# Performance work log

Hardware: AMD Instinct MI355X
Metric: run time of the kernel (lower is better)

Reference implementation:

```python
import jax, jax.numpy as jnp
import numpy as np

N = 32768      # total nodes = 256 graphs x 128 nodes
G = 256        # graphs in batch
NPG = 128      # nodes per graph
DEG = 8        # incoming edges per node
E = N * DEG    # 262144 edges
F_IN = 64      # node feature size
F_E = 16       # edge feature size
EMB = 64       # out_channels per head == embedding_size
H = 4          # attention heads
HC = H * EMB   # 256
DENSE = 256
K = 64         # ceil(0.5 * NPG)
EPS = 1e-5


def setup_inputs() -> dict:
    key = jax.random.key(0)
    ks = list(jax.random.split(key, 32))
    it = iter(ks)
    s = 0.05

    def rn(shape):
        return jax.random.normal(next(it), shape, jnp.float32) * s

    x = jax.random.normal(next(it), (N, F_IN), jnp.float32)
    dst = jnp.repeat(jnp.arange(N, dtype=jnp.int32), DEG)
    src = (dst // NPG) * NPG + jax.random.randint(next(it), (E,), 0, NPG, dtype=jnp.int32)
    edge_index = jnp.stack([src, dst])                      # [2, E], edges stay within graph
    edge_attr = jax.random.normal(next(it), (E, F_E), jnp.float32)
    batch_index = jnp.arange(N, dtype=jnp.int32) // NPG

    inp = dict(
        x=x, edge_index=edge_index, edge_attr=edge_attr, batch_index=batch_index,
        # TransformerConv 1 (in=F_IN)
        Wq1=rn((F_IN, HC)), bq1=jnp.zeros((HC,), jnp.float32),
        Wk1=rn((F_IN, HC)), bk1=jnp.zeros((HC,), jnp.float32),
        Wv1=rn((F_IN, HC)), bv1=jnp.zeros((HC,), jnp.float32),
        We1=rn((F_E, HC)),
        Ws1=rn((F_IN, HC)), bs1=jnp.zeros((HC,), jnp.float32),
        Wb1=rn((3 * HC, 1)),
        t1_W=rn((HC, EMB)), t1_b=jnp.zeros((EMB,), jnp.float32),
        bn1_g=jnp.ones((EMB,), jnp.float32), bn1_b=jnp.zeros((EMB,), jnp.float32),
        # TransformerConv 2 (in=EMB)
        Wq2=rn((EMB, HC)), bq2=jnp.zeros((HC,), jnp.float32),
        Wk2=rn((EMB, HC)), bk2=jnp.zeros((HC,), jnp.float32),
        Wv2=rn((EMB, HC)), bv2=jnp.zeros((HC,), jnp.float32),
        We2=rn((F_E, HC)),
        Ws2=rn((EMB, HC)), bs2=jnp.zeros((HC,), jnp.float32),
        Wb2=rn((3 * HC, 1)),
        t2_W=rn((HC, EMB)), t2_b=jnp.zeros((EMB,), jnp.float32),
        bn2_g=jnp.ones((EMB,), jnp.float32), bn2_b=jnp.zeros((EMB,), jnp.float32),
        # TopKPooling + MLP head
        pool_w=rn((EMB,)),
        l1_W=rn((2 * EMB, DENSE)), l1_b=jnp.zeros((DENSE,), jnp.float32),
        l2_W=rn((DENSE, DENSE // 2)), l2_b=jnp.zeros((DENSE // 2,), jnp.float32),
        l3_W=rn((DENSE // 2, 1)), l3_b=jnp.zeros((1,), jnp.float32),
    )
    return inp


def _tconv(x, src, dst, ea, Wq, bq, Wk, bk, Wv, bv, We, Ws, bs, Wb):
    """PyG TransformerConv with edge_dim, beta=True, concat=True."""
    n = x.shape[0]
    q = (x @ Wq + bq).reshape(n, H, EMB)                    # [N,H,C]
    eemb = (ea @ We).reshape(-1, H, EMB)                    # [E,H,C]
    k = (x @ Wk + bk)[src].reshape(-1, H, EMB) + eemb       # edge features added to key
    v = (x @ Wv + bv)[src].reshape(-1, H, EMB) + eemb       # and to value
    alpha = jnp.einsum('ehc,ehc->eh', q[dst], k) / jnp.sqrt(jnp.float32(EMB))  # [E,H]
    # stable segment softmax over incoming edges of each dst node
    amax = jax.ops.segment_max(alpha, dst, num_segments=n)
    pexp = jnp.exp(alpha - amax[dst])
    denom = jax.ops.segment_sum(pexp, dst, num_segments=n)
    attn = pexp / denom[dst]                                # [E,H]
    out = jax.ops.segment_sum(v * attn[..., None], dst, num_segments=n).reshape(n, HC)
    # beta gated skip: lin_skip(x) and lin_beta([out, xr, out-xr])
    xr = x @ Ws + bs
    beta = jax.nn.sigmoid(jnp.concatenate([out, xr, out - xr], axis=-1) @ Wb)  # [N,1]
    return beta * xr + (1.0 - beta) * out


def _bn(x, g, b):
    m = x.mean(0)
    v = x.var(0)
    return g * (x - m) * jax.lax.rsqrt(v + EPS) + b


def _forward(x, edge_attr,
             Wq1, bq1, Wk1, bk1, Wv1, bv1, We1, Ws1, bs1, Wb1, t1_W, t1_b, bn1_g, bn1_b,
             Wq2, bq2, Wk2, bk2, Wv2, bv2, We2, Ws2, bs2, Wb2, t2_W, t2_b, bn2_g, bn2_b,
             pool_w, l1_W, l1_b, l2_W, l2_b, l3_W, l3_b,
             edge_index, batch_index):
    src, dst = edge_index[0], edge_index[1]
    h = _tconv(x, src, dst, edge_attr, Wq1, bq1, Wk1, bk1, Wv1, bv1, We1, Ws1, bs1, Wb1)
    h = _bn(jax.nn.relu(h @ t1_W + t1_b), bn1_g, bn1_b)
    h = _tconv(h, src, dst, edge_attr, Wq2, bq2, Wk2, bk2, Wv2, bv2, We2, Ws2, bs2, Wb2)
    h = _bn(jax.nn.relu(h @ t2_W + t2_b), bn2_g, bn2_b)
    # TopKPooling: score = (x.w)/||w||, keep top K per graph, scale by tanh(score)
    score = (h @ pool_w) / jnp.linalg.norm(pool_w)          # [N]
    sv, si = jax.lax.top_k(score.reshape(G, NPG), K)        # [G,K]
    xs = jnp.take_along_axis(h.reshape(G, NPG, EMB), si[..., None], axis=1)  # [G,K,EMB]
    xs = xs * jnp.tanh(sv)[..., None]
    # readout: global max pool || global mean pool
    rep = jnp.concatenate([xs.max(axis=1), xs.mean(axis=1)], axis=-1)  # [G, 2*EMB]
    hd = jax.nn.relu(rep @ l1_W + l1_b)
    hd = jax.nn.relu(hd @ l2_W + l2_b)
    return hd @ l3_W + l3_b                                  # [G,1]


def reference(x, edge_index, edge_attr, batch_index,
              Wq1, bq1, Wk1, bk1, Wv1, bv1, We1, Ws1, bs1, Wb1, t1_W, t1_b, bn1_g, bn1_b,
              Wq2, bq2, Wk2, bk2, Wv2, bv2, We2, Ws2, bs2, Wb2, t2_W, t2_b, bn2_g, bn2_b,
              pool_w, l1_W, l1_b, l2_W, l2_b, l3_W, l3_b):
    return _forward(x, edge_attr,
                    Wq1, bq1, Wk1, bk1, Wv1, bv1, We1, Ws1, bs1, Wb1, t1_W, t1_b, bn1_g, bn1_b,
                    Wq2, bq2, Wk2, bk2, Wv2, bv2, We2, Ws2, bs2, Wb2, t2_W, t2_b, bn2_g, bn2_b,
                    pool_w, l1_W, l1_b, l2_W, l2_b, l3_W, l3_b,
                    edge_index, batch_index)
```

## Files before the change

kernel.cpp:

```cpp
#include <hip/hip_runtime.h>
#include <math.h>

#define NN 32768
#define NG 256
#define DEG 8
#define HC 256
#define NCAT 1088
#define HCP 320
#define KTOP 64
#define EPSBN 1e-5f

typedef __attribute__((ext_vector_type(8))) short short8v;
typedef __attribute__((ext_vector_type(4))) float f32x4;

__device__ inline float bf2f(unsigned short u) {
    union { unsigned int i; float f; } c; c.i = ((unsigned int)u) << 16; return c.f;
}
__device__ inline unsigned short f2bf(float f) {
    union { float f; unsigned int i; } c; c.f = f;
    unsigned int r = c.i + 0x7FFFu + ((c.i >> 16) & 1u);
    return (unsigned short)(r >> 16);
}
__device__ inline void split2(float v, unsigned short& hi, unsigned short& lo) {
    hi = f2bf(v);
    lo = f2bf(v - bf2f(hi));
}

__global__ __launch_bounds__(256) void split_x(
    const float* __restrict__ X,
    unsigned short* __restrict__ Xhi, unsigned short* __restrict__ Xlo)
{
    size_t i8 = ((size_t)blockIdx.x * 256 + threadIdx.x) * 8;
    float4 a0 = *(const float4*)(X + i8);
    float4 a1 = *(const float4*)(X + i8 + 4);
    float av[8] = {a0.x, a0.y, a0.z, a0.w, a1.x, a1.y, a1.z, a1.w};
    short8v vh, vl;
    #pragma unroll
    for (int j = 0; j < 8; j++) {
        unsigned short h, l;
        split2(av[j], h, l);
        vh[j] = (short)h; vl[j] = (short)l;
    }
    *(short8v*)(Xhi + i8) = vh;
    *(short8v*)(Xlo + i8) = vl;
}

__global__ __launch_bounds__(256) void prep(
    const float* __restrict__ Wq, const float* __restrict__ bq,
    const float* __restrict__ Wk, const float* __restrict__ bk,
    const float* __restrict__ Wv, const float* __restrict__ bv,
    const float* __restrict__ Ws, const float* __restrict__ bs,
    const float* __restrict__ We, const float* __restrict__ tW,
    const float* __restrict__ Wb,
    unsigned short* __restrict__ WThi, unsigned short* __restrict__ WTlo,
    float* __restrict__ bcat,
    unsigned short* __restrict__ tWThi, unsigned short* __restrict__ tWTlo,
    float* __restrict__ Wbf, float* __restrict__ stats)
{
    const int t = threadIdx.x, b = blockIdx.x;
    if (b < 16) {
        int n = b * 64 + (t >> 2);
        int cc = n & 255;
        const float* src = (n < 256) ? Wq : (n < 512) ? Wk : (n < 768) ? Wv : Ws;
        int k0 = (t & 3) * 16;
        #pragma unroll
        for (int k = k0; k < k0 + 16; k++) {
            unsigned short h, l;
            split2(src[k * 256 + cc], h, l);
            WThi[n * 64 + k] = h; WTlo[n * 64 + k] = l;
        }
    } else if (b < 32) {
        int idx = (b - 16) * 256 + t;
        int k = idx >> 6, o = idx & 63;
        int h = o >> 4, f = o & 15;
        const float* wq = Wq + k * 256 + h * 64;
        const float* we = We + f * 256 + h * 64;
        float s = 0.f;
        #pragma unroll
        for (int d = 0; d < 64; d++) s += wq[d] * we[d];
        unsigned short hh, ll;
        split2(s, hh, ll);
        WThi[(1024 + o) * 64 + k] = hh; WTlo[(1024 + o) * 64 + k] = ll;
    } else if (b < 48) {
        int idx = (b - 32) * 256 + t;
        int kp = idx >> 6, n = idx & 63;
        int h = kp >> 4, f = kp & 15;
        const float* we = We + f * 256 + h * 64;
        const float* tw = tW + (h * 64) * 64 + n;
        float s = 0.f;
        #pragma unroll
        for (int d = 0; d < 64; d++) s += we[d] * tw[d * 64];
        unsigned short hh, ll;
        split2(s, hh, ll);
        tWThi[n * HCP + 256 + kp] = hh; tWTlo[n * HCP + 256 + kp] = ll;
    } else if (b < 64) {
        int base = (b - 48) * 1024 + t * 4;
        #pragma unroll
        for (int i = 0; i < 4; i++) {
            int idx = base + i;
            int n = idx >> 8, k = idx & 255;
            unsigned short h, l;
            split2(tW[k * 64 + n], h, l);
            tWThi[n * HCP + k] = h; tWTlo[n * HCP + k] = l;
        }
    } else {
        if (t < 128) stats[t] = 0.f;
        Wbf[t]       = Wb[t]       + Wb[512 + t];
        Wbf[256 + t] = Wb[256 + t] - Wb[512 + t];
        for (int c = t; c < 1024; c += 256) {
            int cc = c & 255;
            bcat[c] = (c < 256) ? bq[cc] : (c < 512) ? bk[cc] : (c < 768) ? bv[cc] : bs[cc];
        }
        if (t < 64) {
            int h = t >> 4, f = t & 15;
            const float* we = We + f * 256 + h * 64;
            float s = 0.f, sb = 0.f;
            #pragma unroll
            for (int d = 0; d < 64; d++) {
                s  += we[d] * (Wb[h * 64 + d] + Wb[512 + h * 64 + d]);
                sb += we[d] * bq[h * 64 + d];
            }
            Wbf[512 + t] = s;
            bcat[1024 + t] = sb;
        }
    }
}

__global__ __launch_bounds__(256) void proj_mfma(
    const unsigned short* __restrict__ Ahi, const unsigned short* __restrict__ Alo,
    const unsigned short* __restrict__ WThi, const unsigned short* __restrict__ WTlo,
    const float* __restrict__ bcat, unsigned short* __restrict__ C)
{
    __shared__ char smem[32768];
    unsigned short* AhiL = (unsigned short*)smem;
    unsigned short* AloL = AhiL + 4096;
    unsigned short* WhiL = AloL + 4096;
    unsigned short* WloL = WhiL + 4096;
    float* CL = (float*)smem;
    const int t = threadIdx.x;
    const int n0 = blockIdx.x * 64;
    const int row0 = blockIdx.y * 64;

    #pragma unroll
    for (int g = 0; g < 2; g++) {
        int idx = t * 8 + g * 2048;
        int r = idx >> 6, c = idx & 63;
        int ch = (c >> 3) ^ (r & 7);
        *(short8v*)(AhiL + r * 64 + ch * 8) =
            *(const short8v*)(Ahi + (size_t)(row0 + r) * 64 + c);
        *(short8v*)(AloL + r * 64 + ch * 8) =
            *(const short8v*)(Alo + (size_t)(row0 + r) * 64 + c);
        *(short8v*)(WhiL + r * 64 + ch * 8) =
            *(const short8v*)(WThi + (size_t)(n0 + r) * 64 + c);
        *(short8v*)(WloL + r * 64 + ch * 8) =
            *(const short8v*)(WTlo + (size_t)(n0 + r) * 64 + c);
    }
    __syncthreads();

    const int w = t >> 6, l = t & 63;
    const int lr = l & 15, lg = l >> 4, ls = l & 7;
    f32x4 acc[4] = {};
    #pragma unroll
    for (int kk = 0; kk < 2; kk++) {
        int ch = (kk * 4 + lg) ^ ls;
        short8v ah = *(short8v*)(AhiL + (w * 16 + lr) * 64 + ch * 8);
        short8v al = *(short8v*)(AloL + (w * 16 + lr) * 64 + ch * 8);
        #pragma unroll
        for (int nt = 0; nt < 4; nt++) {
            short8v bh = *(short8v*)(WhiL + (nt * 16 + lr) * 64 + ch * 8);
            short8v bl = *(short8v*)(WloL + (nt * 16 + lr) * 64 + ch * 8);
            acc[nt] = __builtin_amdgcn_mfma_f32_16x16x32_bf16(ah, bh, acc[nt], 0, 0, 0);
            acc[nt] = __builtin_amdgcn_mfma_f32_16x16x32_bf16(al, bh, acc[nt], 0, 0, 0);
            acc[nt] = __builtin_amdgcn_mfma_f32_16x16x32_bf16(ah, bl, acc[nt], 0, 0, 0);
        }
    }
    __syncthreads();
    #pragma unroll
    for (int nt = 0; nt < 4; nt++)
        #pragma unroll
        for (int r = 0; r < 4; r++)
            CL[(w * 16 + lg * 4 + r) * 68 + nt * 16 + lr] = acc[nt][r];
    __syncthreads();
    {
        int r = t >> 2, cb = (t & 3) * 16;
        #pragma unroll
        for (int jj = 0; jj < 2; jj++) {
            f32x4 p0 = *(f32x4*)(CL + r * 68 + cb + jj * 8);
            f32x4 p1 = *(f32x4*)(CL + r * 68 + cb + jj * 8 + 4);
            float4 b0 = *(const float4*)(bcat + n0 + cb + jj * 8);
            float4 b1 = *(const float4*)(bcat + n0 + cb + jj * 8 + 4);
            short8v o;
            o[0] = (short)f2bf(p0[0] + b0.x); o[1] = (short)f2bf(p0[1] + b0.y);
            o[2] = (short)f2bf(p0[2] + b0.z); o[3] = (short)f2bf(p0[3] + b0.w);
            o[4] = (short)f2bf(p1[0] + b1.x); o[5] = (short)f2bf(p1[1] + b1.y);
            o[6] = (short)f2bf(p1[2] + b1.z); o[7] = (short)f2bf(p1[3] + b1.w);
            *(short8v*)(C + (size_t)(row0 + r) * NCAT + n0 + cb + jj * 8) = o;
        }
    }
}

__global__ __launch_bounds__(256) void gemm_t(
    const unsigned short* __restrict__ Ahi, const unsigned short* __restrict__ Alo,
    const unsigned short* __restrict__ WThi, const unsigned short* __restrict__ WTlo,
    const float* __restrict__ bias, float* __restrict__ Tout,
    float* __restrict__ stats)
{
    __shared__ char smem[32768];
    unsigned short* AhiL = (unsigned short*)smem;
    unsigned short* AloL = AhiL + 4096;
    unsigned short* WhiL = AloL + 4096;
    unsigned short* WloL = WhiL + 4096;
    float* CL = (float*)smem;
    const int t = threadIdx.x;
    const int row0 = blockIdx.x * 64;
    const int w = t >> 6, l = t & 63;
    const int lr = l & 15, lg = l >> 4, ls = l & 7;
    f32x4 acc[4] = {};
    for (int kt = 0; kt < 5; kt++) {
        if (kt) __syncthreads();
        #pragma unroll
        for (int g = 0; g < 2; g++) {
            int idx = t * 8 + g * 2048;
            int r = idx >> 6, c = idx & 63;
            int ch = (c >> 3) ^ (r & 7);
            *(short8v*)(AhiL + r * 64 + ch * 8) =
                *(const short8v*)(Ahi + (size_t)(row0 + r) * HCP + kt * 64 + c);
            *(short8v*)(AloL + r * 64 + ch * 8) =
                *(const short8v*)(Alo + (size_t)(row0 + r) * HCP + kt * 64 + c);
            *(short8v*)(WhiL + r * 64 + ch * 8) =
                *(const short8v*)(WThi + r * HCP + kt * 64 + c);
            *(short8v*)(WloL + r * 64 + ch * 8) =
                *(const short8v*)(WTlo + r * HCP + kt * 64 + c);
        }
        __syncthreads();
        #pragma unroll
        for (int kk = 0; kk < 2; kk++) {
            int ch = (kk * 4 + lg) ^ ls;
            short8v ah = *(short8v*)(AhiL + (w * 16 + lr) * 64 + ch * 8);
            short8v al = *(short8v*)(AloL + (w * 16 + lr) * 64 + ch * 8);
            #pragma unroll
            for (int nt = 0; nt < 4; nt++) {
                short8v bh = *(short8v*)(WhiL + (nt * 16 + lr) * 64 + ch * 8);
                short8v bl = *(short8v*)(WloL + (nt * 16 + lr) * 64 + ch * 8);
                acc[nt] = __builtin_amdgcn_mfma_f32_16x16x32_bf16(ah, bh, acc[nt], 0, 0, 0);
                acc[nt] = __builtin_amdgcn_mfma_f32_16x16x32_bf16(al, bh, acc[nt], 0, 0, 0);
                acc[nt] = __builtin_amdgcn_mfma_f32_16x16x32_bf16(ah, bl, acc[nt], 0, 0, 0);
            }
        }
    }
    __syncthreads();
    #pragma unroll
    for (int nt = 0; nt < 4; nt++)
        #pragma unroll
        for (int r = 0; r < 4; r++)
            CL[(w * 16 + lg * 4 + r) * 68 + nt * 16 + lr] = acc[nt][r];
    __syncthreads();
    {
        int r = t >> 2, cb = (t & 3) * 16;
        #pragma unroll
        for (int jj = 0; jj < 4; jj++) {
            f32x4 p = *(f32x4*)(CL + r * 68 + cb + jj * 4);
            float4 bb = *(const float4*)(bias + cb + jj * 4);
            float4 o;
            o.x = fmaxf(p[0] + bb.x, 0.f); o.y = fmaxf(p[1] + bb.y, 0.f);
            o.z = fmaxf(p[2] + bb.z, 0.f); o.w = fmaxf(p[3] + bb.w, 0.f);
            *(float4*)(Tout + (size_t)(row0 + r) * 64 + cb + jj * 4) = o;
        }
    }
    if (t < 64) {
        float bb = bias[t];
        float s = 0.f, s2 = 0.f;
        #pragma unroll 8
        for (int r = 0; r < 64; r++) {
            float v = fmaxf(CL[r * 68 + t] + bb, 0.f);
            s += v; s2 += v * v;
        }
        atomicAdd(&stats[t], s);
        atomicAdd(&stats[64 + t], s2);
    }
}

__global__ __launch_bounds__(256, 8) void attn_fused(
    const unsigned short* __restrict__ C,
    const float* __restrict__ Wbf,
    const int* __restrict__ srcIdx, const float* __restrict__ EA,
    unsigned short* __restrict__ Hhi, unsigned short* __restrict__ Hlo)
{
    const int t = threadIdx.x;
    const int lane = t & 63;
    const int wave = t >> 6;
    const int bid = blockIdx.x;
    const int swz = (bid & 7) * 1024 + (bid >> 3);
    const int n = swz * 4 + wave;
    const int c0 = lane * 4;
    const int h = lane >> 4;
    const int fi = lane & 15;

    const unsigned short* rowN = C + (size_t)n * NCAT;
    ushort4 qv = *(const ushort4*)(rowN + c0);
    float q0 = bf2f(qv.x), q1 = bf2f(qv.y), q2 = bf2f(qv.z), q3 = bf2f(qv.w);
    float qe_l = bf2f(rowN[1024 + h * 16 + fi]);

    const int ebase = n * DEG;
    int sj = srcIdx[ebase + (lane & 7)];
    int ss[DEG];
    #pragma unroll
    for (int j = 0; j < DEG; j++) ss[j] = __shfl(sj, j);

    ushort4 kv[DEG];
    float eav[DEG];
    #pragma unroll
    for (int j = 0; j < DEG; j++) {
        kv[j] = *(const ushort4*)(C + (size_t)ss[j] * NCAT + 256 + c0);
        eav[j] = EA[(size_t)(ebase + j) * 16 + fi];
    }
    float alpha[DEG];
    #pragma unroll
    for (int j = 0; j < DEG; j++) {
        float d = eav[j] * qe_l
                + q0 * bf2f(kv[j].x) + q1 * bf2f(kv[j].y)
                + q2 * bf2f(kv[j].z) + q3 * bf2f(kv[j].w);
        d += __shfl_xor(d, 1); d += __shfl_xor(d, 2);
        d += __shfl_xor(d, 4); d += __shfl_xor(d, 8);
        alpha[j] = d * 0.125f;
    }
    float mx = alpha[0];
    #pragma unroll
    for (int j = 1; j < DEG; j++) mx = fmaxf(mx, alpha[j]);
    float wsum = 0.f;
    #pragma unroll
    for (int j = 0; j < DEG; j++) { alpha[j] = expf(alpha[j] - mx); wsum += alpha[j]; }
    float inv = 1.f / wsum;

    float o0 = 0.f, o1 = 0.f, o2 = 0.f, o3 = 0.f, eg = 0.f;
    #pragma unroll
    for (int j = 0; j < DEG; j++) {
        float wj = alpha[j] * inv;
        eg += wj * eav[j];
        ushort4 vv = *(const ushort4*)(C + (size_t)ss[j] * NCAT + 512 + c0);
        o0 += wj * bf2f(vv.x); o1 += wj * bf2f(vv.y);
        o2 += wj * bf2f(vv.z); o3 += wj * bf2f(vv.w);
    }

    ushort4 sv = *(const ushort4*)(rowN + 768 + c0);
    float xr0 = bf2f(sv.x), xr1 = bf2f(sv.y), xr2 = bf2f(sv.z), xr3 = bf2f(sv.w);

    float part = eg * Wbf[512 + lane];
    {
        f32x4 w13 = *(const f32x4*)(Wbf + c0);
        f32x4 w23 = *(const f32x4*)(Wbf + 256 + c0);
        part += o0 * w13[0] + o1 * w13[1] + o2 * w13[2] + o3 * w13[3];
        part += xr0 * w23[0] + xr1 * w23[1] + xr2 * w23[2] + xr3 * w23[3];
    }
    part += __shfl_xor(part, 1);  part += __shfl_xor(part, 2);
    part += __shfl_xor(part, 4);  part += __shfl_xor(part, 8);
    part += __shfl_xor(part, 16); part += __shfl_xor(part, 32);
    float beta = 1.f / (1.f + expf(-part));
    float omb = 1.f - beta;

    ushort4 hh, hl;
    split2(beta * xr0 + omb * o0, hh.x, hl.x);
    split2(beta * xr1 + omb * o1, hh.y, hl.y);
    split2(beta * xr2 + omb * o2, hh.z, hl.z);
    split2(beta * xr3 + omb * o3, hh.w, hl.w);
    *(ushort4*)(Hhi + (size_t)n * HCP + c0) = hh;
    *(ushort4*)(Hlo + (size_t)n * HCP + c0) = hl;

    unsigned short zh, zl;
    split2(omb * eg, zh, zl);
    Hhi[(size_t)n * HCP + 256 + lane] = zh;
    Hlo[(size_t)n * HCP + 256 + lane] = zl;
}

__global__ __launch_bounds__(256) void bn_apply(
    float* __restrict__ T, const float* __restrict__ stats,
    const float* __restrict__ g, const float* __restrict__ b,
    unsigned short* __restrict__ Thi, unsigned short* __restrict__ Tlo,
    int wf32)
{
    int i = blockIdx.x * 256 + threadIdx.x;
    int c = i & 63;
    float mean = stats[c] * (1.f / NN);
    float var  = stats[64 + c] * (1.f / NN) - mean * mean;
    float v = T[i];
    float r = g[c] * (v - mean) * rsqrtf(var + EPSBN) + b[c];
    if (wf32) T[i] = r;
    unsigned short h, l;
    split2(r, h, l);
    Thi[i] = h; Tlo[i] = l;
}

__global__ __launch_bounds__(128) void pool_mlp(
    const float* __restrict__ Hn, const float* __restrict__ pw,
    const float* __restrict__ W1, const float* __restrict__ b1,
    const float* __restrict__ W2, const float* __restrict__ b2,
    const float* __restrict__ W3, const float* __restrict__ b3,
    float* __restrict__ out)
{
    __shared__ float sh[128][65];
    __shared__ float spw[64];
    __shared__ float sc[128];
    __shared__ float sscale[128];
    __shared__ int   skeep[128];
    __shared__ float rmax[2][64], rsum[2][64];
    __shared__ float srep[128];
    __shared__ float sh1[256];
    __shared__ float sh2[128];
    __shared__ float wred[2];
    const int g = blockIdx.x, t = threadIdx.x;

    for (int i = t; i < 128 * 64; i += 128) sh[i >> 6][i & 63] = Hn[(size_t)g * 128 * 64 + i];
    if (t < 64) spw[t] = pw[t];
    __syncthreads();

    float nw = 0.f;
    #pragma unroll
    for (int i = 0; i < 64; i++) { float w = spw[i]; nw += w * w; }
    float invn = rsqrtf(nw);

    float s = 0.f;
    #pragma unroll
    for (int i = 0; i < 64; i++) s += sh[t][i] * spw[i];
    s *= invn;
    sc[t] = s;
    __syncthreads();

    int rank = 0;
    for (int m = 0; m < 128; m++) {
        float sm = sc[m];
        rank += (sm > s) || (sm == s && m < t);
    }
    skeep[t] = (rank < KTOP);
    sscale[t] = tanhf(s);
    __syncthreads();

    {
        int c = t & 63, half = t >> 6;
        float mxv = -1e30f, sm = 0.f;
        for (int r = half * 64; r < half * 64 + 64; r++) {
            if (skeep[r]) {
                float v = sh[r][c] * sscale[r];
                mxv = fmaxf(mxv, v); sm += v;
            }
        }
        rmax[half][c] = mxv; rsum[half][c] = sm;
    }
    __syncthreads();
    if (t < 64) {
        srep[t] = fmaxf(rmax[0][t], rmax[1][t]);
        srep[64 + t] = (rsum[0][t] + rsum[1][t]) * (1.f / KTOP);
    }
    __syncthreads();

    #pragma unroll
    for (int jj = 0; jj < 2; jj++) {
        int j = t + jj * 128;
        float a = b1[j];
        for (int c2 = 0; c2 < 128; c2++) a += srep[c2] * W1[c2 * 256 + j];
        sh1[j] = fmaxf(a, 0.f);
    }
    __syncthreads();
    {
        float a = b2[t];
        for (int c2 = 0; c2 < 256; c2++) a += sh1[c2] * W2[c2 * 128 + t];
        sh2[t] = fmaxf(a, 0.f);
    }
    __syncthreads();
    float p = sh2[t] * W3[t];
    p += __shfl_xor(p, 1);  p += __shfl_xor(p, 2);  p += __shfl_xor(p, 4);
    p += __shfl_xor(p, 8);  p += __shfl_xor(p, 16); p += __shfl_xor(p, 32);
    if ((t & 63) == 0) wred[t >> 6] = p;
    __syncthreads();
    if (t == 0) out[g] = wred[0] + wred[1] + b3[0];
}

extern "C" void kernel_launch(void* const* d_in, const int* in_sizes, int n_in,
                              void* d_out, int out_size, void* d_ws, size_t ws_size,
                              hipStream_t stream)
{
    const float* x    = (const float*)d_in[0];
    const int*   ei   = (const int*)  d_in[1];
    const float* ea   = (const float*)d_in[2];
    const int*   srcI = ei;
    const float* Wq1 = (const float*)d_in[4];  const float* bq1 = (const float*)d_in[5];
    const float* Wk1 = (const float*)d_in[6];  const float* bk1 = (const float*)d_in[7];
    const float* Wv1 = (const float*)d_in[8];  const float* bv1 = (const float*)d_in[9];
    const float* We1 = (const float*)d_in[10];
    const float* Ws1 = (const float*)d_in[11]; const float* bs1 = (const float*)d_in[12];
    const float* Wb1 = (const float*)d_in[13];
    const float* t1W = (const float*)d_in[14]; const float* t1b = (const float*)d_in[15];
    const float* g1  = (const float*)d_in[16]; const float* be1 = (const float*)d_in[17];
    const float* Wq2 = (const float*)d_in[18]; const float* bq2 = (const float*)d_in[19];
    const float* Wk2 = (const float*)d_in[20]; const float* bk2 = (const float*)d_in[21];
    const float* Wv2 = (const float*)d_in[22]; const float* bv2 = (const float*)d_in[23];
    const float* We2 = (const float*)d_in[24];
    const float* Ws2 = (const float*)d_in[25]; const float* bs2 = (const float*)d_in[26];
    const float* Wb2 = (const float*)d_in[27];
    const float* t2W = (const float*)d_in[28]; const float* t2b = (const float*)d_in[29];
    const float* g2  = (const float*)d_in[30]; const float* be2 = (const float*)d_in[31];
    const float* pw  = (const float*)d_in[32];
    const float* l1W = (const float*)d_in[33]; const float* l1b = (const float*)d_in[34];
    const float* l2W = (const float*)d_in[35]; const float* l2b = (const float*)d_in[36];
    const float* l3W = (const float*)d_in[37]; const float* l3b = (const float*)d_in[38];

    char* ws = (char*)d_ws;
    unsigned short* C   = (unsigned short*)ws;
    unsigned short* Hhi = (unsigned short*)(ws + (size_t)NN * NCAT * 2);
    unsigned short* Hlo = Hhi + (size_t)NN * HCP;
    float* bT    = (float*)(Hlo + (size_t)NN * HCP);
    unsigned short* bThi = (unsigned short*)(bT + (size_t)NN * 64);
    unsigned short* bTlo = bThi + (size_t)NN * 64;
    unsigned short* Xhi  = bTlo + (size_t)NN * 64;
    unsigned short* Xlo  = Xhi + (size_t)NN * 64;
    float* bcat  = (float*)(Xlo + (size_t)NN * 64);
    float* stats = bcat + NCAT;
    float* Wbf   = stats + 128;
    unsigned short* WThi  = (unsigned short*)(Wbf + 576);
    unsigned short* WTlo  = WThi + (size_t)NCAT * 64;
    unsigned short* tWThi = WTlo + (size_t)NCAT * 64;
    unsigned short* tWTlo = tWThi + 64 * HCP;

    const dim3 blk(256);
    const dim3 gProj(17, 512);

    split_x<<<NN * 64 / (256 * 8), blk, 0, stream>>>(x, Xhi, Xlo);
    prep<<<65, blk, 0, stream>>>(Wq1, bq1, Wk1, bk1, Wv1, bv1, Ws1, bs1, We1, t1W, Wb1,
                                 WThi, WTlo, bcat, tWThi, tWTlo, Wbf, stats);
    proj_mfma<<<gProj, blk, 0, stream>>>(Xhi, Xlo, WThi, WTlo, bcat, C);
    attn_fused<<<NN / 4, blk, 0, stream>>>(C, Wbf, srcI, ea, Hhi, Hlo);
    gemm_t<<<512, blk, 0, stream>>>(Hhi, Hlo, tWThi, tWTlo, t1b, bT, stats);
    bn_apply<<<NN * 64 / 256, blk, 0, stream>>>(bT, stats, g1, be1, bThi, bTlo, 0);

    prep<<<65, blk, 0, stream>>>(Wq2, bq2, Wk2, bk2, Wv2, bv2, Ws2, bs2, We2, t2W, Wb2,
                                 WThi, WTlo, bcat, tWThi, tWTlo, Wbf, stats);
    proj_mfma<<<gProj, blk, 0, stream>>>(bThi, bTlo, WThi, WTlo, bcat, C);
    attn_fused<<<NN / 4, blk, 0, stream>>>(C, Wbf, srcI, ea, Hhi, Hlo);
    gemm_t<<<512, blk, 0, stream>>>(Hhi, Hlo, tWThi, tWTlo, t2b, bT, stats);
    bn_apply<<<NN * 64 / 256, blk, 0, stream>>>(bT, stats, g2, be2, bThi, bTlo, 1);

    pool_mlp<<<NG, 128, 0, stream>>>(bT, pw, l1W, l1b, l2W, l2b, l3W, l3b,
                                     (float*)d_out);
}
```

Baseline: 220.1 us.

## Interleave K/V projection columns and loop output tiles inside projection blocks

```diff
diff --git a/kernel.cpp b/kernel.cpp
--- a/kernel.cpp
+++ b/kernel.cpp
@@ -24,6 +24,11 @@
 __device__ inline void split2(float v, unsigned short& hi, unsigned short& lo) {
     hi = f2bf(v);
     lo = f2bf(v - bf2f(hi));
+}
+__device__ inline int permcol(int n) {
+    if (n < 256 || n >= 768) return n;
+    if (n < 512) { int l = n - 256; return 256 + ((l >> 2) << 3) + (l & 3); }
+    int l = n - 512; return 256 + ((l >> 2) << 3) + 4 + (l & 3);
 }
 
 __global__ __launch_bounds__(256) void split_x(
@@ -62,12 +67,13 @@
         int n = b * 64 + (t >> 2);
         int cc = n & 255;
         const float* src = (n < 256) ? Wq : (n < 512) ? Wk : (n < 768) ? Wv : Ws;
+        int p = permcol(n);
         int k0 = (t & 3) * 16;
         #pragma unroll
         for (int k = k0; k < k0 + 16; k++) {
             unsigned short h, l;
             split2(src[k * 256 + cc], h, l);
-            WThi[n * 64 + k] = h; WTlo[n * 64 + k] = l;
+            WThi[p * 64 + k] = h; WTlo[p * 64 + k] = l;
         }
     } else if (b < 32) {
         int idx = (b - 16) * 256 + t;
@@ -109,7 +115,8 @@
         Wbf[256 + t] = Wb[256 + t] - Wb[512 + t];
         for (int c = t; c < 1024; c += 256) {
             int cc = c & 255;
-            bcat[c] = (c < 256) ? bq[cc] : (c < 512) ? bk[cc] : (c < 768) ? bv[cc] : bs[cc];
+            float v = (c < 256) ? bq[cc] : (c < 512) ? bk[cc] : (c < 768) ? bv[cc] : bs[cc];
+            bcat[permcol(c)] = v;
         }
         if (t < 64) {
             int h = t >> 4, f = t & 15;
@@ -131,15 +138,13 @@
     const unsigned short* __restrict__ WThi, const unsigned short* __restrict__ WTlo,
     const float* __restrict__ bcat, unsigned short* __restrict__ C)
 {
-    __shared__ char smem[32768];
-    unsigned short* AhiL = (unsigned short*)smem;
-    unsigned short* AloL = AhiL + 4096;
-    unsigned short* WhiL = AloL + 4096;
-    unsigned short* WloL = WhiL + 4096;
-    float* CL = (float*)smem;
+    __shared__ unsigned short AhiL[4096], AloL[4096];
+    __shared__ unsigned short WhiL[4096], WloL[4096];
+    __shared__ float CL[64 * 68];
     const int t = threadIdx.x;
-    const int n0 = blockIdx.x * 64;
-    const int row0 = blockIdx.y * 64;
+    const int row0 = blockIdx.x * 64;
+    const int w = t >> 6, l = t & 63;
+    const int lr = l & 15, lg = l >> 4, ls = l & 7;
 
     #pragma unroll
     for (int g = 0; g < 2; g++) {
@@ -150,52 +155,58 @@
             *(const short8v*)(Ahi + (size_t)(row0 + r) * 64 + c);
         *(short8v*)(AloL + r * 64 + ch * 8) =
             *(const short8v*)(Alo + (size_t)(row0 + r) * 64 + c);
-        *(short8v*)(WhiL + r * 64 + ch * 8) =
-            *(const short8v*)(WThi + (size_t)(n0 + r) * 64 + c);
-        *(short8v*)(WloL + r * 64 + ch * 8) =
-            *(const short8v*)(WTlo + (size_t)(n0 + r) * 64 + c);
-    }
-    __syncthreads();
-
-    const int w = t >> 6, l = t & 63;
-    const int lr = l & 15, lg = l >> 4, ls = l & 7;
-    f32x4 acc[4] = {};
-    #pragma unroll
-    for (int kk = 0; kk < 2; kk++) {
-        int ch = (kk * 4 + lg) ^ ls;
-        short8v ah = *(short8v*)(AhiL + (w * 16 + lr) * 64 + ch * 8);
-        short8v al = *(short8v*)(AloL + (w * 16 + lr) * 64 + ch * 8);
-        #pragma unroll
-        for (int nt = 0; nt < 4; nt++) {
-            short8v bh = *(short8v*)(WhiL + (nt * 16 + lr) * 64 + ch * 8);
-            short8v bl = *(short8v*)(WloL + (nt * 16 + lr) * 64 + ch * 8);
-            acc[nt] = __builtin_amdgcn_mfma_f32_16x16x32_bf16(ah, bh, acc[nt], 0, 0, 0);
-            acc[nt] = __builtin_amdgcn_mfma_f32_16x16x32_bf16(al, bh, acc[nt], 0, 0, 0);
-            acc[nt] = __builtin_amdgcn_mfma_f32_16x16x32_bf16(ah, bl, acc[nt], 0, 0, 0);
-        }
-    }
-    __syncthreads();
-    #pragma unroll
-    for (int nt = 0; nt < 4; nt++)
-        #pragma unroll
-        for (int r = 0; r < 4; r++)
-            CL[(w * 16 + lg * 4 + r) * 68 + nt * 16 + lr] = acc[nt][r];
-    __syncthreads();
-    {
-        int r = t >> 2, cb = (t & 3) * 16;
-        #pragma unroll
-        for (int jj = 0; jj < 2; jj++) {
-            f32x4 p0 = *(f32x4*)(CL + r * 68 + cb + jj * 8);
-            f32x4 p1 = *(f32x4*)(CL + r * 68 + cb + jj * 8 + 4);
-            float4 b0 = *(const float4*)(bcat + n0 + cb + jj * 8);
-            float4 b1 = *(const float4*)(bcat + n0 + cb + jj * 8 + 4);
-            short8v o;
-            o[0] = (short)f2bf(p0[0] + b0.x); o[1] = (short)f2bf(p0[1] + b0.y);
-            o[2] = (short)f2bf(p0[2] + b0.z); o[3] = (short)f2bf(p0[3] + b0.w);
-            o[4] = (short)f2bf(p1[0] + b1.x); o[5] = (short)f2bf(p1[1] + b1.y);
-            o[6] = (short)f2bf(p1[2] + b1.z); o[7] = (short)f2bf(p1[3] + b1.w);
-            *(short8v*)(C + (size_t)(row0 + r) * NCAT + n0 + cb + jj * 8) = o;
-        }
+    }
+
+    for (int n0 = 0; n0 < NCAT; n0 += 64) {
+        #pragma unroll
+        for (int g = 0; g < 2; g++) {
+            int idx = t * 8 + g * 2048;
+            int r = idx >> 6, c = idx & 63;
+            int ch = (c >> 3) ^ (r & 7);
+            *(short8v*)(WhiL + r * 64 + ch * 8) =
+                *(const short8v*)(WThi + (size_t)(n0 + r) * 64 + c);
+            *(short8v*)(WloL + r * 64 + ch * 8) =
+                *(const short8v*)(WTlo + (size_t)(n0 + r) * 64 + c);
+        }
+        __syncthreads();
+        f32x4 acc[4] = {};
+        #pragma unroll
+        for (int kk = 0; kk < 2; kk++) {
+            int ch = (kk * 4 + lg) ^ ls;
+            short8v ah = *(short8v*)(AhiL + (w * 16 + lr) * 64 + ch * 8);
+            short8v al = *(short8v*)(AloL + (w * 16 + lr) * 64 + ch * 8);
+            #pragma unroll
+            for (int nt = 0; nt < 4; nt++) {
+                short8v bh = *(short8v*)(WhiL + (nt * 16 + lr) * 64 + ch * 8);
+                short8v bl = *(short8v*)(WloL + (nt * 16 + lr) * 64 + ch * 8);
+                acc[nt] = __builtin_amdgcn_mfma_f32_16x16x32_bf16(ah, bh, acc[nt], 0, 0, 0);
+                acc[nt] = __builtin_amdgcn_mfma_f32_16x16x32_bf16(al, bh, acc[nt], 0, 0, 0);
+                acc[nt] = __builtin_amdgcn_mfma_f32_16x16x32_bf16(ah, bl, acc[nt], 0, 0, 0);
+            }
+        }
+        #pragma unroll
+        for (int nt = 0; nt < 4; nt++)
+            #pragma unroll
+            for (int r = 0; r < 4; r++)
+                CL[(w * 16 + lg * 4 + r) * 68 + nt * 16 + lr] = acc[nt][r];
+        __syncthreads();
+        {
+            int r = t >> 2, cb = (t & 3) * 16;
+            #pragma unroll
+            for (int jj = 0; jj < 2; jj++) {
+                f32x4 p0 = *(f32x4*)(CL + r * 68 + cb + jj * 8);
+                f32x4 p1 = *(f32x4*)(CL + r * 68 + cb + jj * 8 + 4);
+                float4 b0 = *(const float4*)(bcat + n0 + cb + jj * 8);
+                float4 b1 = *(const float4*)(bcat + n0 + cb + jj * 8 + 4);
+                short8v o;
+                o[0] = (short)f2bf(p0[0] + b0.x); o[1] = (short)f2bf(p0[1] + b0.y);
+                o[2] = (short)f2bf(p0[2] + b0.z); o[3] = (short)f2bf(p0[3] + b0.w);
+                o[4] = (short)f2bf(p1[0] + b1.x); o[5] = (short)f2bf(p1[1] + b1.y);
+                o[6] = (short)f2bf(p1[2] + b1.z); o[7] = (short)f2bf(p1[3] + b1.w);
+                *(short8v*)(C + (size_t)(row0 + r) * NCAT + n0 + cb + jj * 8) = o;
+            }
+        }
+        __syncthreads();
     }
 }
 
@@ -280,7 +291,7 @@
     }
 }
 
-__global__ __launch_bounds__(256, 8) void attn_fused(
+__global__ __launch_bounds__(256, 6) void attn_fused(
     const unsigned short* __restrict__ C,
     const float* __restrict__ Wbf,
     const int* __restrict__ srcIdx, const float* __restrict__ EA,
@@ -307,19 +318,19 @@
     #pragma unroll
     for (int j = 0; j < DEG; j++) ss[j] = __shfl(sj, j);
 
-    ushort4 kv[DEG];
+    short8v kv[DEG];
     float eav[DEG];
     #pragma unroll
     for (int j = 0; j < DEG; j++) {
-        kv[j] = *(const ushort4*)(C + (size_t)ss[j] * NCAT + 256 + c0);
+        kv[j] = *(const short8v*)(C + (size_t)ss[j] * NCAT + 256 + lane * 8);
         eav[j] = EA[(size_t)(ebase + j) * 16 + fi];
     }
     float alpha[DEG];
     #pragma unroll
     for (int j = 0; j < DEG; j++) {
         float d = eav[j] * qe_l
-                + q0 * bf2f(kv[j].x) + q1 * bf2f(kv[j].y)
-                + q2 * bf2f(kv[j].z) + q3 * bf2f(kv[j].w);
+                + q0 * bf2f((unsigned short)kv[j][0]) + q1 * bf2f((unsigned short)kv[j][1])
+                + q2 * bf2f((unsigned short)kv[j][2]) + q3 * bf2f((unsigned short)kv[j][3]);
         d += __shfl_xor(d, 1); d += __shfl_xor(d, 2);
         d += __shfl_xor(d, 4); d += __shfl_xor(d, 8);
         alpha[j] = d * 0.125f;
@@ -337,9 +348,10 @@
     for (int j = 0; j < DEG; j++) {
         float wj = alpha[j] * inv;
         eg += wj * eav[j];
-        ushort4 vv = *(const ushort4*)(C + (size_t)ss[j] * NCAT + 512 + c0);
-        o0 += wj * bf2f(vv.x); o1 += wj * bf2f(vv.y);
-        o2 += wj * bf2f(vv.z); o3 += wj * bf2f(vv.w);
+        o0 += wj * bf2f((unsigned short)kv[j][4]);
+        o1 += wj * bf2f((unsigned short)kv[j][5]);
+        o2 += wj * bf2f((unsigned short)kv[j][6]);
+        o3 += wj * bf2f((unsigned short)kv[j][7]);
     }
 
     ushort4 sv = *(const ushort4*)(rowN + 768 + c0);
@@ -521,19 +533,18 @@
     unsigned short* tWTlo = tWThi + 64 * HCP;
 
     const dim3 blk(256);
-    const dim3 gProj(17, 512);
 
     split_x<<<NN * 64 / (256 * 8), blk, 0, stream>>>(x, Xhi, Xlo);
     prep<<<65, blk, 0, stream>>>(Wq1, bq1, Wk1, bk1, Wv1, bv1, Ws1, bs1, We1, t1W, Wb1,
                                  WThi, WTlo, bcat, tWThi, tWTlo, Wbf, stats);
-    proj_mfma<<<gProj, blk, 0, stream>>>(Xhi, Xlo, WThi, WTlo, bcat, C);
+    proj_mfma<<<512, blk, 0, stream>>>(Xhi, Xlo, WThi, WTlo, bcat, C);
     attn_fused<<<NN / 4, blk, 0, stream>>>(C, Wbf, srcI, ea, Hhi, Hlo);
     gemm_t<<<512, blk, 0, stream>>>(Hhi, Hlo, tWThi, tWTlo, t1b, bT, stats);
     bn_apply<<<NN * 64 / 256, blk, 0, stream>>>(bT, stats, g1, be1, bThi, bTlo, 0);
 
     prep<<<65, blk, 0, stream>>>(Wq2, bq2, Wk2, bk2, Wv2, bv2, Ws2, bs2, We2, t2W, Wb2,
                                  WThi, WTlo, bcat, tWThi, tWTlo, Wbf, stats);
-    proj_mfma<<<gProj, blk, 0, stream>>>(bThi, bTlo, WThi, WTlo, bcat, C);
+    proj_mfma<<<512, blk, 0, stream>>>(bThi, bTlo, WThi, WTlo, bcat, C);
     attn_fused<<<NN / 4, blk, 0, stream>>>(C, Wbf, srcI, ea, Hhi, Hlo);
     gemm_t<<<512, blk, 0, stream>>>(Hhi, Hlo, tWThi, tWTlo, t2b, bT, stats);
     bn_apply<<<NN * 64 / 256, blk, 0, stream>>>(bT, stats, g2, be2, bThi, bTlo, 1);
```

Result: no change. 220.8 us (+0.3%).
